# Performance work log

Hardware: AMD Instinct MI355X
Metric: run time of the kernel (lower is better)

## Reference

```python
import jax, jax.numpy as jnp
import numpy as np


def setup_inputs() -> dict:
    key = jax.random.key(0)
    ks = jax.random.split(key, 5)
    B, C, D, H, W = 8, 128, 4, 128, 128
    x = jax.random.normal(ks[0], (B, C, D, H, W), dtype=jnp.float32)
    # Conv3d(depth, depth, kernel_size=1) on a 1x1x1 input == linear over channels.
    w1 = jax.random.normal(ks[1], (C, C), dtype=jnp.float32) * (1.0 / np.sqrt(C))
    b1 = jax.random.normal(ks[2], (C,), dtype=jnp.float32) * 0.01
    w2 = jax.random.normal(ks[3], (C, C), dtype=jnp.float32) * (1.0 / np.sqrt(C))
    b2 = jax.random.normal(ks[4], (C,), dtype=jnp.float32) * 0.01
    return {"x": x, "w1": w1, "b1": b1, "w2": w2, "b2": b2}


def reference(x, w1, b1, w2, b2):
    # AdaptiveMaxPool3d(1): global max over D,H,W -> [B, C]
    gp = jnp.max(x, axis=(2, 3, 4))
    # 1x1 conv -> ReLU -> 1x1 conv -> Sigmoid  (all per-channel linear on [B, C])
    h = jax.nn.relu(jnp.einsum('bc,oc->bo', gp, w1) + b1)
    g = jax.nn.sigmoid(jnp.einsum('bc,oc->bo', h, w2) + b2)
    # The torch.cat chain just tiles the gate to [B, C, 4, iter, iter];
    # equivalent to a broadcast multiply.
    return x * g[:, :, None, None, None]
```

## Files before the change

### kernel.cpp

```cpp
#include <hip/hip_runtime.h>
#include <math.h>

#define CCH 128
#define BB  8
#define DHW 65536

typedef float f4 __attribute__((ext_vector_type(4)));

__global__ __launch_bounds__(256) void pool_max_kernel(
    const float* __restrict__ x, float* __restrict__ gp) {
    const int bc  = blockIdx.x;
    const int tid = threadIdx.x;
    const f4* xp = (const f4*)x + (size_t)bc * (DHW / 4);

    float m = -INFINITY;
#pragma unroll 8
    for (int k = 0; k < 64; ++k) {
        f4 v = __builtin_nontemporal_load(&xp[tid + k * 256]);
        m = fmaxf(m, fmaxf(fmaxf(v.x, v.y), fmaxf(v.z, v.w)));
    }
#pragma unroll
    for (int off = 32; off > 0; off >>= 1)
        m = fmaxf(m, __shfl_down(m, off, 64));

    __shared__ float sm[4];
    const int wave = tid >> 6, lane = tid & 63;
    if (lane == 0) sm[wave] = m;
    __syncthreads();
    if (tid == 0)
        gp[bc] = fmaxf(fmaxf(sm[0], sm[1]), fmaxf(sm[2], sm[3]));
}

__global__ __launch_bounds__(128) void fc_kernel(
    const float* __restrict__ gp,
    const float* __restrict__ w1, const float* __restrict__ b1,
    const float* __restrict__ w2, const float* __restrict__ b2,
    float* __restrict__ g) {
    __shared__ float sgp[BB][CCH];
    __shared__ float sh[BB][CCH];
    const int o = threadIdx.x;

#pragma unroll
    for (int b = 0; b < BB; ++b) sgp[b][o] = gp[b * CCH + o];
    __syncthreads();

    float acc[BB];
#pragma unroll
    for (int b = 0; b < BB; ++b) acc[b] = b1[o];
    for (int c = 0; c < CCH; ++c) {
        const float w = w1[o * CCH + c];
#pragma unroll
        for (int b = 0; b < BB; ++b) acc[b] += sgp[b][c] * w;
    }
#pragma unroll
    for (int b = 0; b < BB; ++b) sh[b][o] = fmaxf(acc[b], 0.0f);
    __syncthreads();

#pragma unroll
    for (int b = 0; b < BB; ++b) acc[b] = b2[o];
    for (int c = 0; c < CCH; ++c) {
        const float w = w2[o * CCH + c];
#pragma unroll
        for (int b = 0; b < BB; ++b) acc[b] += sh[b][c] * w;
    }
#pragma unroll
    for (int b = 0; b < BB; ++b)
        g[b * CCH + o] = 1.0f / (1.0f + expf(-acc[b]));
}

__global__ __launch_bounds__(256) void scale_kernel(
    const float* __restrict__ x, const float* __restrict__ g,
    float* __restrict__ out) {
    const int bc   = blockIdx.x >> 2;
    const int part = blockIdx.x & 3;
    const float gate = g[bc];
    const size_t base = (size_t)bc * (DHW / 4) + (size_t)part * 4096;
    const f4* xp = (const f4*)x + base;
    f4*       op = (f4*)out + base;
    const int tid = threadIdx.x;
#pragma unroll
    for (int k = 0; k < 16; ++k) {
        f4 v = __builtin_nontemporal_load(&xp[tid + k * 256]);
        v *= gate;
        __builtin_nontemporal_store(v, &op[tid + k * 256]);
    }
}

extern "C" void kernel_launch(void* const* d_in, const int* in_sizes, int n_in,
                              void* d_out, int out_size, void* d_ws, size_t ws_size,
                              hipStream_t stream) {
    const float* x  = (const float*)d_in[0];
    const float* w1 = (const float*)d_in[1];
    const float* b1 = (const float*)d_in[2];
    const float* w2 = (const float*)d_in[3];
    const float* b2 = (const float*)d_in[4];
    float* out = (float*)d_out;

    float* gp = (float*)d_ws;
    float* g  = gp + BB * CCH;

    pool_max_kernel<<<BB * CCH, 256, 0, stream>>>(x, gp);
    fc_kernel<<<1, CCH, 0, stream>>>(gp, w1, b1, w2, b2, g);
    scale_kernel<<<BB * CCH * 4, 256, 0, stream>>>(x, g, out);
}
```

Before: 484.7 us.

## Fuse pool, FC and scale into one cooperative kernel keeping slab on-chip

Replaces the three-kernel pipeline with a single cooperative-grid kernel. Each block reduces the max over its channel slab while caching part of the slab in registers and LDS, then syncs the whole grid, computes its own gate from the FC layers, and scales the cached data without reloading it from HBM. The remaining part of the slab is reloaded from memory. This removes two launches and cuts global reads of x by roughly 40%, at the cost of a grid-wide barrier, heavy register pressure, and redundant FC work in every block. If the cooperative launch fails, the code falls back to the original three kernels.

```diff
diff --git a/kernel.cpp b/kernel.cpp
--- a/kernel.cpp
+++ b/kernel.cpp
@@ -1,18 +1,124 @@
 #include <hip/hip_runtime.h>
+#include <hip/hip_cooperative_groups.h>
 #include <math.h>
+
+namespace cg = cooperative_groups;
 
 #define CCH 128
 #define BB  8
+#define SLAB 16384
 #define DHW 65536
+#define NREG 18
+#define NLDS 9
+#define NSTREAM (64 - NREG - NLDS)
 
 typedef float f4 __attribute__((ext_vector_type(4)));
+
+__global__ __launch_bounds__(256, 4) void fused_kernel(
+    const float* __restrict__ x,
+    const float* __restrict__ w1, const float* __restrict__ b1,
+    const float* __restrict__ w2, const float* __restrict__ b2,
+    float* __restrict__ out, float* __restrict__ gp)
+{
+    __shared__ f4    lx[NLDS * 256];
+    __shared__ float h[CCH];
+    __shared__ float red[4];
+    __shared__ float gsh;
+
+    const int bc  = blockIdx.x;
+    const int tid = threadIdx.x;
+    const f4* xp = (const f4*)x + (size_t)bc * SLAB + tid;
+
+    f4 r[NREG];
+    float a0 = -INFINITY, a1 = -INFINITY, a2 = -INFINITY, a3 = -INFINITY;
+
+#pragma unroll
+    for (int k = 0; k < NREG; ++k) {
+        f4 v = __builtin_nontemporal_load(&xp[k * 256]);
+        r[k] = v;
+        float mm = fmaxf(fmaxf(v.x, v.y), fmaxf(v.z, v.w));
+        if ((k & 3) == 0) a0 = fmaxf(a0, mm);
+        else if ((k & 3) == 1) a1 = fmaxf(a1, mm);
+        else if ((k & 3) == 2) a2 = fmaxf(a2, mm);
+        else a3 = fmaxf(a3, mm);
+    }
+#pragma unroll
+    for (int k = 0; k < NLDS; ++k) {
+        f4 v = __builtin_nontemporal_load(&xp[(NREG + k) * 256]);
+        lx[tid + k * 256] = v;
+        float mm = fmaxf(fmaxf(v.x, v.y), fmaxf(v.z, v.w));
+        if ((k & 3) == 0) a0 = fmaxf(a0, mm);
+        else if ((k & 3) == 1) a1 = fmaxf(a1, mm);
+        else if ((k & 3) == 2) a2 = fmaxf(a2, mm);
+        else a3 = fmaxf(a3, mm);
+    }
+#pragma unroll 8
+    for (int k = 0; k < NSTREAM; ++k) {
+        f4 v = __builtin_nontemporal_load(&xp[(NREG + NLDS + k) * 256]);
+        float mm = fmaxf(fmaxf(v.x, v.y), fmaxf(v.z, v.w));
+        if ((k & 3) == 0) a0 = fmaxf(a0, mm);
+        else if ((k & 3) == 1) a1 = fmaxf(a1, mm);
+        else if ((k & 3) == 2) a2 = fmaxf(a2, mm);
+        else a3 = fmaxf(a3, mm);
+    }
+    float m = fmaxf(fmaxf(a0, a1), fmaxf(a2, a3));
+#pragma unroll
+    for (int off = 32; off > 0; off >>= 1)
+        m = fmaxf(m, __shfl_down(m, off, 64));
+    const int wave = tid >> 6, lane = tid & 63;
+    if (lane == 0) red[wave] = m;
+    __syncthreads();
+    if (tid == 0) {
+        gp[bc] = fmaxf(fmaxf(red[0], red[1]), fmaxf(red[2], red[3]));
+        __threadfence();
+    }
+
+    cg::this_grid().sync();
+
+    const int b = bc >> 7, c = bc & 127;
+    if (tid < CCH) {
+        float acc = b1[tid];
+        const float* wr  = w1 + tid * CCH;
+        const float* gpb = gp + b * CCH;
+#pragma unroll 8
+        for (int j = 0; j < CCH; ++j) acc += wr[j] * gpb[j];
+        h[tid] = fmaxf(acc, 0.0f);
+    }
+    __syncthreads();
+    float p = 0.0f;
+    if (tid < CCH) p = w2[c * CCH + tid] * h[tid];
+#pragma unroll
+    for (int off = 32; off > 0; off >>= 1) p += __shfl_down(p, off, 64);
+    if (lane == 0) red[wave] = p;
+    __syncthreads();
+    if (tid == 0) gsh = 1.0f / (1.0f + expf(-(b2[c] + red[0] + red[1])));
+    __syncthreads();
+    const float gate = gsh;
+
+    f4* op = (f4*)out + (size_t)bc * SLAB + tid;
+#pragma unroll
+    for (int k = 0; k < NREG; ++k) {
+        f4 v = r[k]; v *= gate;
+        __builtin_nontemporal_store(v, &op[k * 256]);
+    }
+#pragma unroll
+    for (int k = 0; k < NLDS; ++k) {
+        f4 v = lx[tid + k * 256]; v *= gate;
+        __builtin_nontemporal_store(v, &op[(NREG + k) * 256]);
+    }
+#pragma unroll 8
+    for (int k = 0; k < NSTREAM; ++k) {
+        f4 v = __builtin_nontemporal_load(&xp[(NREG + NLDS + k) * 256]);
+        v *= gate;
+        __builtin_nontemporal_store(v, &op[(NREG + NLDS + k) * 256]);
+    }
+}
 
 __global__ __launch_bounds__(256) void pool_max_kernel(
     const float* __restrict__ x, float* __restrict__ gp) {
     const int bc  = blockIdx.x;
     const int tid = threadIdx.x;
     const f4* xp = (const f4*)x + (size_t)bc * (DHW / 4);
-
     float m = -INFINITY;
 #pragma unroll 8
     for (int k = 0; k < 64; ++k) {
@@ -22,7 +128,6 @@
 #pragma unroll
     for (int off = 32; off > 0; off >>= 1)
         m = fmaxf(m, __shfl_down(m, off, 64));
-
     __shared__ float sm[4];
     const int wave = tid >> 6, lane = tid & 63;
     if (lane == 0) sm[wave] = m;
@@ -39,11 +144,9 @@
     __shared__ float sgp[BB][CCH];
     __shared__ float sh[BB][CCH];
     const int o = threadIdx.x;
-
 #pragma unroll
     for (int b = 0; b < BB; ++b) sgp[b][o] = gp[b * CCH + o];
     __syncthreads();
-
     float acc[BB];
 #pragma unroll
     for (int b = 0; b < BB; ++b) acc[b] = b1[o];
@@ -55,7 +158,6 @@
 #pragma unroll
     for (int b = 0; b < BB; ++b) sh[b][o] = fmaxf(acc[b], 0.0f);
     __syncthreads();
-
 #pragma unroll
     for (int b = 0; b < BB; ++b) acc[b] = b2[o];
     for (int c = 0; c < CCH; ++c) {
@@ -95,11 +197,17 @@
     const float* w2 = (const float*)d_in[3];
     const float* b2 = (const float*)d_in[4];
     float* out = (float*)d_out;
-
-    float* gp = (float*)d_ws;
-    float* g  = gp + BB * CCH;
-
-    pool_max_kernel<<<BB * CCH, 256, 0, stream>>>(x, gp);
-    fc_kernel<<<1, CCH, 0, stream>>>(gp, w1, b1, w2, b2, g);
-    scale_kernel<<<BB * CCH * 4, 256, 0, stream>>>(x, g, out);
-}
+    float* gp  = (float*)d_ws;
+    float* g   = gp + BB * CCH;
+
+    void* args[] = { (void*)&x, (void*)&w1, (void*)&b1, (void*)&w2,
+                     (void*)&b2, (void*)&out, (void*)&gp };
+    hipError_t err = hipLaunchCooperativeKernel(
+        (const void*)fused_kernel, dim3(BB * CCH), dim3(256), args, 0, stream);
+
+    if (err != hipSuccess) {
+        pool_max_kernel<<<BB * CCH, 256, 0, stream>>>(x, gp);
+        fc_kernel<<<1, CCH, 0, stream>>>(gp, w1, b1, w2, b2, g);
+        scale_kernel<<<BB * CCH * 4, 256, 0, stream>>>(x, g, out);
+    }
+}
```

Result: slower. 624.8 us (+28.9%).

## Fuse FC gate computation into scale kernel and widen pooling blocks

Applied to the files above, without the earlier changes.

Removes the single-block FC kernel launch by having every scale block recompute the hidden layer for its batch and the dot product for its channel, then apply the gate. This eliminates one serialized launch plus a tiny one-block kernel between the two bandwidth-bound passes, at the cost of redundant FC work (a 128x128 matvec per block) before streaming starts. The pooling kernel also moves to 512 threads with four independent max accumulators to increase memory-level parallelism.

```diff
diff --git a/kernel.cpp b/kernel.cpp
--- a/kernel.cpp
+++ b/kernel.cpp
@@ -3,81 +3,84 @@
 
 #define CCH 128
 #define BB  8
-#define DHW 65536
+#define SLAB 16384
 
 typedef float f4 __attribute__((ext_vector_type(4)));
 
-__global__ __launch_bounds__(256) void pool_max_kernel(
+__global__ __launch_bounds__(512) void pool_max_kernel(
     const float* __restrict__ x, float* __restrict__ gp) {
     const int bc  = blockIdx.x;
     const int tid = threadIdx.x;
-    const f4* xp = (const f4*)x + (size_t)bc * (DHW / 4);
+    const f4* xp = (const f4*)x + (size_t)bc * SLAB + tid;
 
-    float m = -INFINITY;
+    float a0 = -INFINITY, a1 = -INFINITY, a2 = -INFINITY, a3 = -INFINITY;
 #pragma unroll 8
-    for (int k = 0; k < 64; ++k) {
-        f4 v = __builtin_nontemporal_load(&xp[tid + k * 256]);
-        m = fmaxf(m, fmaxf(fmaxf(v.x, v.y), fmaxf(v.z, v.w)));
+    for (int k = 0; k < 32; ++k) {
+        f4 v = __builtin_nontemporal_load(&xp[k * 512]);
+        float mm = fmaxf(fmaxf(v.x, v.y), fmaxf(v.z, v.w));
+        if ((k & 3) == 0) a0 = fmaxf(a0, mm);
+        else if ((k & 3) == 1) a1 = fmaxf(a1, mm);
+        else if ((k & 3) == 2) a2 = fmaxf(a2, mm);
+        else a3 = fmaxf(a3, mm);
     }
+    float m = fmaxf(fmaxf(a0, a1), fmaxf(a2, a3));
 #pragma unroll
     for (int off = 32; off > 0; off >>= 1)
         m = fmaxf(m, __shfl_down(m, off, 64));
 
-    __shared__ float sm[4];
+    __shared__ float sm[8];
     const int wave = tid >> 6, lane = tid & 63;
     if (lane == 0) sm[wave] = m;
     __syncthreads();
-    if (tid == 0)
-        gp[bc] = fmaxf(fmaxf(sm[0], sm[1]), fmaxf(sm[2], sm[3]));
+    if (tid == 0) {
+        float r = sm[0];
+#pragma unroll
+        for (int w = 1; w < 8; ++w) r = fmaxf(r, sm[w]);
+        gp[bc] = r;
+    }
 }
 
-__global__ __launch_bounds__(128) void fc_kernel(
-    const float* __restrict__ gp,
+__global__ __launch_bounds__(256) void scale_fc_kernel(
+    const float* __restrict__ x,  const float* __restrict__ gp,
     const float* __restrict__ w1, const float* __restrict__ b1,
     const float* __restrict__ w2, const float* __restrict__ b2,
-    float* __restrict__ g) {
-    __shared__ float sgp[BB][CCH];
-    __shared__ float sh[BB][CCH];
-    const int o = threadIdx.x;
-
-#pragma unroll
-    for (int b = 0; b < BB; ++b) sgp[b][o] = gp[b * CCH + o];
-    __syncthreads();
-
-    float acc[BB];
-#pragma unroll
-    for (int b = 0; b < BB; ++b) acc[b] = b1[o];
-    for (int c = 0; c < CCH; ++c) {
-        const float w = w1[o * CCH + c];
-#pragma unroll
-        for (int b = 0; b < BB; ++b) acc[b] += sgp[b][c] * w;
-    }
-#pragma unroll
-    for (int b = 0; b < BB; ++b) sh[b][o] = fmaxf(acc[b], 0.0f);
-    __syncthreads();
-
-#pragma unroll
-    for (int b = 0; b < BB; ++b) acc[b] = b2[o];
-    for (int c = 0; c < CCH; ++c) {
-        const float w = w2[o * CCH + c];
-#pragma unroll
-        for (int b = 0; b < BB; ++b) acc[b] += sh[b][c] * w;
-    }
-#pragma unroll
-    for (int b = 0; b < BB; ++b)
-        g[b * CCH + o] = 1.0f / (1.0f + expf(-acc[b]));
-}
-
-__global__ __launch_bounds__(256) void scale_kernel(
-    const float* __restrict__ x, const float* __restrict__ g,
     float* __restrict__ out) {
     const int bc   = blockIdx.x >> 2;
     const int part = blockIdx.x & 3;
-    const float gate = g[bc];
-    const size_t base = (size_t)bc * (DHW / 4) + (size_t)part * 4096;
+    const int b = bc >> 7, c = bc & 127;
+    const int tid = threadIdx.x;
+
+    __shared__ float h[CCH];
+    __shared__ float red[4];
+    __shared__ float gsh;
+
+    if (tid < CCH) {
+        float acc = b1[tid];
+        const f4* wr = (const f4*)(w1 + tid * CCH);
+        const f4* gb = (const f4*)(gp + b * CCH);
+#pragma unroll 8
+        for (int j = 0; j < CCH / 4; ++j) {
+            f4 wv = wr[j], gv = gb[j];
+            acc += wv.x * gv.x + wv.y * gv.y + wv.z * gv.z + wv.w * gv.w;
+        }
+        h[tid] = fmaxf(acc, 0.0f);
+    }
+    __syncthreads();
+
+    float p = 0.0f;
+    if (tid < CCH) p = w2[c * CCH + tid] * h[tid];
+#pragma unroll
+    for (int off = 32; off > 0; off >>= 1) p += __shfl_down(p, off, 64);
+    const int wave = tid >> 6, lane = tid & 63;
+    if (lane == 0) red[wave] = p;
+    __syncthreads();
+    if (tid == 0) gsh = 1.0f / (1.0f + expf(-(b2[c] + red[0] + red[1])));
+    __syncthreads();
+    const float gate = gsh;
+
+    const size_t base = (size_t)bc * SLAB + (size_t)part * 4096;
     const f4* xp = (const f4*)x + base;
     f4*       op = (f4*)out + base;
-    const int tid = threadIdx.x;
 #pragma unroll
     for (int k = 0; k < 16; ++k) {
         f4 v = __builtin_nontemporal_load(&xp[tid + k * 256]);
@@ -95,11 +98,8 @@
     const float* w2 = (const float*)d_in[3];
     const float* b2 = (const float*)d_in[4];
     float* out = (float*)d_out;
+    float* gp  = (float*)d_ws;
 
-    float* gp = (float*)d_ws;
-    float* g  = gp + BB * CCH;
-
-    pool_max_kernel<<<BB * CCH, 256, 0, stream>>>(x, gp);
-    fc_kernel<<<1, CCH, 0, stream>>>(gp, w1, b1, w2, b2, g);
-    scale_kernel<<<BB * CCH * 4, 256, 0, stream>>>(x, g, out);
+    pool_max_kernel<<<BB * CCH, 512, 0, stream>>>(x, gp);
+    scale_fc_kernel<<<BB * CCH * 4, 256, 0, stream>>>(x, gp, w1, b1, w2, b2, out);
 }
```

New measurement: 487.0 us. No clear change (+0.5%).
